# Kernel optimization log

Measured on AMD Instinct MI355X. Metric: run time of the kernel, lower is better.

Reference implementation:

```python
import jax, jax.numpy as jnp
import numpy as np

N_NODES = 50000
N_EDGES = 800000
IN_F = 128
HID_F = 128
OUT_F = 128

def safediv(a, b):
    b = jnp.where(b == 0, jnp.ones_like(b), b)
    return a / b

def setup_inputs() -> dict:
    key = jax.random.key(0)
    ks = jax.random.split(key, 8)
    h = jax.random.normal(ks[0], (N_NODES, IN_F), dtype=jnp.float32)
    ppr_weight = jax.random.uniform(ks[1], (N_EDGES,), dtype=jnp.float32)
    Qw = jax.random.normal(ks[2], (HID_F, IN_F), dtype=jnp.float32) * (1.0 / np.sqrt(IN_F))
    Qb = jnp.zeros((HID_F,), dtype=jnp.float32)
    Ww = jax.random.normal(ks[3], (OUT_F, IN_F + HID_F), dtype=jnp.float32) * (1.0 / np.sqrt(IN_F + HID_F))
    Wb = jnp.zeros((OUT_F,), dtype=jnp.float32)
    src = jax.random.randint(ks[4], (N_EDGES,), 0, N_NODES, dtype=jnp.int64 if jax.config.jax_enable_x64 else jnp.int32)
    dst = jax.random.randint(ks[5], (N_EDGES,), 0, N_NODES, dtype=jnp.int64 if jax.config.jax_enable_x64 else jnp.int32)
    return {"h": h, "ppr_weight": ppr_weight, "Qw": Qw, "Qb": Qb, "Ww": Ww, "Wb": Wb, "src": src, "dst": dst}

def reference(h, ppr_weight, Qw, Qb, Ww, Wb, src, dst):
    # neighbor transform: Q(h) -> [N, HID_F]
    hq = h @ Qw.T + Qb
    # message: h_w = hq[src] * ppr_weight  (edge-weighted gather) [E, HID_F]
    msg = hq[src] * ppr_weight[:, None]
    # reduce: scatter-sum messages and weights onto dst nodes
    h_agg = jax.ops.segment_sum(msg, dst, num_segments=N_NODES)
    w = jax.ops.segment_sum(ppr_weight, dst, num_segments=N_NODES)
    # apply: PPR-weighted mean, concat, linear, leaky_relu, L2 normalize
    h_agg = safediv(h_agg, w[:, None])
    h_concat = jnp.concatenate([h, h_agg], axis=1)
    h_new = jax.nn.leaky_relu(h_concat @ Ww.T + Wb, negative_slope=0.01)
    norm = jnp.linalg.norm(h_new, axis=1, keepdims=True)
    return safediv(h_new, norm)
```

## Files before the change

### kernel.cpp

```cpp
#include <hip/hip_runtime.h>
#include <stdint.h>

#define N_NODES 50000
#define N_EDGES 800000
#define IN_F 128
#define HID_F 128
#define OUT_F 128
#define CAT_F 256
#define N_STRIPS 3125

#define NB 64
#define NBUCK 782
#define CHUNK_E (N_EDGES / NB)
#define SLEN (NBUCK * NB)
#define BCAP 1280

typedef __bf16 bf16x8 __attribute__((ext_vector_type(8)));
typedef float f32x4 __attribute__((ext_vector_type(4)));

union BF8 {
  bf16x8 v;
  uint16_t u[8];
};

__device__ __forceinline__ uint32_t f2b(float f) {
  uint32_t u = __float_as_uint(f);
  return (u + 0x7fffu + ((u >> 16) & 1u)) >> 16;
}

__global__ void __launch_bounds__(256) prep_hist_kernel(
    const int* __restrict__ dst, int* __restrict__ G,
    const float* __restrict__ Qw, const float* __restrict__ Ww,
    uint16_t* __restrict__ QwB, uint16_t* __restrict__ WwB) {
  if (blockIdx.x < NB) {
    __shared__ int hist[NBUCK];
    for (int k = threadIdx.x; k < NBUCK; k += 256) hist[k] = 0;
    __syncthreads();
    int base = blockIdx.x * CHUNK_E;
    for (int e = base + threadIdx.x; e < base + CHUNK_E; e += 256)
      atomicAdd(&hist[dst[e] >> 6], 1);
    __syncthreads();
    for (int k = threadIdx.x; k < NBUCK; k += 256)
      G[k * NB + blockIdx.x] = hist[k];
  } else {
    const int TOT4 = (HID_F * IN_F + OUT_F * CAT_F) / 4;
    int i4 = (blockIdx.x - NB) * 256 + threadIdx.x;
    if (i4 >= TOT4) return;
    int base = i4 * 4;
    const float* src;
    uint16_t* dstp;
    int off;
    if (base < HID_F * IN_F) {
      src = Qw; dstp = QwB; off = base;
    } else {
      src = Ww; dstp = WwB; off = base - HID_F * IN_F;
    }
    float4 v = *(const float4*)(src + off);
    ushort4 o;
    o.x = (uint16_t)f2b(v.x); o.y = (uint16_t)f2b(v.y);
    o.z = (uint16_t)f2b(v.z); o.w = (uint16_t)f2b(v.w);
    *(ushort4*)(dstp + off) = o;
  }
}

__global__ void __launch_bounds__(1024) scan_kernel(const int* __restrict__ G,
                                                    int* __restrict__ offs) {
  __shared__ int wsum[17];
  int t = threadIdx.x;
  int lane = t & 63;
  int wv = t >> 6;
  int base = 0;
  for (int chunk = 0; chunk < 7; ++chunk) {
    int idx0 = chunk * 8192 + t * 8;
    int c[8];
    if (idx0 + 8 <= SLEN) {
      int4 v0 = *(const int4*)(G + idx0);
      int4 v1 = *(const int4*)(G + idx0 + 4);
      c[0] = v0.x; c[1] = v0.y; c[2] = v0.z; c[3] = v0.w;
      c[4] = v1.x; c[5] = v1.y; c[6] = v1.z; c[7] = v1.w;
    } else {
#pragma unroll
      for (int j = 0; j < 8; ++j) c[j] = (idx0 + j < SLEN) ? G[idx0 + j] : 0;
    }
    int loc[8];
    int s = 0;
#pragma unroll
    for (int j = 0; j < 8; ++j) {
      loc[j] = s;
      s += c[j];
    }
    int inc = s;
#pragma unroll
    for (int d = 1; d < 64; d <<= 1) {
      int v = __shfl_up(inc, d, 64);
      if (lane >= d) inc += v;
    }
    if (lane == 63) wsum[wv] = inc;
    __syncthreads();
    if (wv == 0) {
      int x = (lane < 16) ? wsum[lane] : 0;
      int xi = x;
#pragma unroll
      for (int d = 1; d < 16; d <<= 1) {
        int v = __shfl_up(xi, d, 64);
        if (lane >= d) xi += v;
      }
      if (lane < 16) wsum[lane] = xi - x;
      if (lane == 15) wsum[16] = xi;
    }
    __syncthreads();
    int texc = base + wsum[wv] + (inc - s);
    int ctot = wsum[16];
#pragma unroll
    for (int j = 0; j < 8; ++j) {
      int i = idx0 + j;
      if (i <= SLEN) offs[i] = texc + loc[j];
    }
    base += ctot;
    __syncthreads();
  }
}

__device__ __forceinline__ void gemm1_body(int gb, const float* __restrict__ h,
                                           const uint16_t* __restrict__ QwB,
                                           const float* __restrict__ Qb,
                                           uint16_t* __restrict__ hqB) {
  int wave = (gb * 256 + (int)threadIdx.x) >> 6;
  if (wave >= N_STRIPS) return;
  int lane = threadIdx.x & 63;
  int r = lane & 15, qd = lane >> 4;
  int row0 = wave * 16;
  f32x4 acc[8];
#pragma unroll
  for (int t = 0; t < 8; ++t) acc[t] = (f32x4){0.f, 0.f, 0.f, 0.f};
  const float* aRow = h + (size_t)(row0 + r) * IN_F + qd * 8;
#pragma unroll
  for (int kt = 0; kt < 4; ++kt) {
    float4 v0 = *(const float4*)(aRow + kt * 32);
    float4 v1 = *(const float4*)(aRow + kt * 32 + 4);
    BF8 a;
    a.u[0] = (uint16_t)f2b(v0.x); a.u[1] = (uint16_t)f2b(v0.y);
    a.u[2] = (uint16_t)f2b(v0.z); a.u[3] = (uint16_t)f2b(v0.w);
    a.u[4] = (uint16_t)f2b(v1.x); a.u[5] = (uint16_t)f2b(v1.y);
    a.u[6] = (uint16_t)f2b(v1.z); a.u[7] = (uint16_t)f2b(v1.w);
#pragma unroll
    for (int t = 0; t < 8; ++t) {
      bf16x8 b = *(const bf16x8*)(QwB + (t * 16 + r) * IN_F + kt * 32 + qd * 8);
      acc[t] = __builtin_amdgcn_mfma_f32_16x16x32_bf16(a.v, b, acc[t], 0, 0, 0);
    }
  }
#pragma unroll
  for (int t = 0; t < 8; ++t) {
    float qb = Qb[t * 16 + r];
#pragma unroll
    for (int rr = 0; rr < 4; ++rr) {
      int m = row0 + qd * 4 + rr;
      hqB[(size_t)m * HID_F + t * 16 + r] = (uint16_t)f2b(acc[t][rr] + qb);
    }
  }
}

__global__ void __launch_bounds__(256) scatter_gemm1_kernel(
    const int* __restrict__ dst, const int* __restrict__ src, const float* __restrict__ ppr,
    const int* __restrict__ offs, int2* __restrict__ rec, const float* __restrict__ h,
    const uint16_t* __restrict__ QwB, const float* __restrict__ Qb,
    uint16_t* __restrict__ hqB) {
  if (blockIdx.x < NB) {
    __shared__ int cursor[NBUCK];
    int b = blockIdx.x;
    for (int k = threadIdx.x; k < NBUCK; k += 256) cursor[k] = offs[k * NB + b];
    __syncthreads();
    int base = b * CHUNK_E;
    for (int e = base + threadIdx.x; e < base + CHUNK_E; e += 256) {
      int d = dst[e];
      int s = src[e];
      float w = ppr[e];
      int pos = atomicAdd(&cursor[d >> 6], 1);
      rec[pos] = make_int2(s | ((d & 63) << 20), __float_as_int(w));
    }
  } else {
    gemm1_body(blockIdx.x - NB, h, QwB, Qb, hqB);
  }
}

__global__ void __launch_bounds__(256) aggregate_kernel(const uint16_t* __restrict__ hqB,
                                                        const int2* __restrict__ rec,
                                                        const int* __restrict__ offs,
                                                        uint16_t* __restrict__ haggB) {
  __shared__ int2 srec[BCAP];
  __shared__ int hist[64];
  __shared__ int noff[65];
  __shared__ int cur[64];
  int g = blockIdx.x;
  int t = threadIdx.x;
  if (t < 64) hist[t] = 0;
  __syncthreads();

  int rbeg = offs[g * NB];
  int rend = offs[(g + 1) * NB];
  int len = rend - rbeg;

  for (int i = t; i < len; i += 256) {
    int2 rc = rec[rbeg + i];
    atomicAdd(&hist[rc.x >> 20], 1);
  }
  __syncthreads();

  if (t < 64) {
    int v = hist[t];
    int inc = v;
#pragma unroll
    for (int d = 1; d < 64; d <<= 1) {
      int x = __shfl_up(inc, d, 64);
      if (t >= d) inc += x;
    }
    noff[t] = inc - v;
    cur[t] = inc - v;
    if (t == 63) noff[64] = inc;
  }
  __syncthreads();

  for (int i = t; i < len; i += 256) {
    int2 rc = rec[rbeg + i];
    int p = atomicAdd(&cur[rc.x >> 20], 1);
    if (p < BCAP) srec[p] = rc;
  }
  __syncthreads();

  int lane = t & 63, wv = t >> 6;
  int sub = lane >> 4, c = lane & 15;
  const uint4* hq4 = (const uint4*)hqB;
  for (int nl = wv * 16; nl < wv * 16 + 16; ++nl) {
    int node = g * 64 + nl;
    if (node >= N_NODES) continue;
    int nbeg = noff[nl], nend = noff[nl + 1];
    int m = nend - nbeg;
    float a[8];
#pragma unroll
    for (int j = 0; j < 8; ++j) a[j] = 0.f;
    float ws = 0.f;
    if (m > 0) {
      int last = nend - 1;
      for (int e0 = nbeg; e0 < nend; e0 += 16) {
        int2 rc[4];
#pragma unroll
        for (int q = 0; q < 4; ++q) {
          int i = e0 + q * 4 + sub;
          rc[q] = srec[(i < last) ? i : last];
        }
        uint4 u[4];
#pragma unroll
        for (int q = 0; q < 4; ++q) u[q] = hq4[(size_t)(rc[q].x & 0xFFFFF) * 16 + c];
#pragma unroll
        for (int q = 0; q < 4; ++q) {
          float w = (e0 + q * 4 + sub <= last) ? __int_as_float(rc[q].y) : 0.f;
          ws += w;
          uint32_t x;
          x = u[q].x;
          a[0] += w * __uint_as_float(x << 16);
          a[1] += w * __uint_as_float(x & 0xffff0000u);
          x = u[q].y;
          a[2] += w * __uint_as_float(x << 16);
          a[3] += w * __uint_as_float(x & 0xffff0000u);
          x = u[q].z;
          a[4] += w * __uint_as_float(x << 16);
          a[5] += w * __uint_as_float(x & 0xffff0000u);
          x = u[q].w;
          a[6] += w * __uint_as_float(x << 16);
          a[7] += w * __uint_as_float(x & 0xffff0000u);
        }
      }
    }
#pragma unroll
    for (int j = 0; j < 8; ++j) {
      a[j] += __shfl_xor(a[j], 16);
      a[j] += __shfl_xor(a[j], 32);
    }
    ws += __shfl_xor(ws, 16);
    ws += __shfl_xor(ws, 32);
    float dnm = (ws == 0.f) ? 1.f : ws;
    float inv = 1.f / dnm;
    if (sub == 0) {
      uint4 o;
      o.x = f2b(a[0] * inv) | (f2b(a[1] * inv) << 16);
      o.y = f2b(a[2] * inv) | (f2b(a[3] * inv) << 16);
      o.z = f2b(a[4] * inv) | (f2b(a[5] * inv) << 16);
      o.w = f2b(a[6] * inv) | (f2b(a[7] * inv) << 16);
      ((uint4*)haggB)[(size_t)node * 16 + c] = o;
    }
  }
}

__global__ void __launch_bounds__(256) gemm2_kernel(const float* __restrict__ h,
                                                    const uint16_t* __restrict__ haggB,
                                                    const uint16_t* __restrict__ WwB,
                                                    const float* __restrict__ Wb,
                                                    float* __restrict__ out) {
  int wave = (blockIdx.x * 256 + (int)threadIdx.x) >> 6;
  if (wave >= N_STRIPS) return;
  int lane = threadIdx.x & 63;
  int r = lane & 15, qd = lane >> 4;
  int row0 = wave * 16;
  f32x4 acc[8];
#pragma unroll
  for (int t = 0; t < 8; ++t) acc[t] = (f32x4){0.f, 0.f, 0.f, 0.f};
  const float* aRow = h + (size_t)(row0 + r) * IN_F + qd * 8;
#pragma unroll
  for (int kt = 0; kt < 8; ++kt) {
    bf16x8 av;
    if (kt < 4) {
      float4 v0 = *(const float4*)(aRow + kt * 32);
      float4 v1 = *(const float4*)(aRow + kt * 32 + 4);
      BF8 ab;
      ab.u[0] = (uint16_t)f2b(v0.x); ab.u[1] = (uint16_t)f2b(v0.y);
      ab.u[2] = (uint16_t)f2b(v0.z); ab.u[3] = (uint16_t)f2b(v0.w);
      ab.u[4] = (uint16_t)f2b(v1.x); ab.u[5] = (uint16_t)f2b(v1.y);
      ab.u[6] = (uint16_t)f2b(v1.z); ab.u[7] = (uint16_t)f2b(v1.w);
      av = ab.v;
    } else {
      av = *(const bf16x8*)(haggB + (size_t)(row0 + r) * HID_F + (kt - 4) * 32 + qd * 8);
    }
#pragma unroll
    for (int t = 0; t < 8; ++t) {
      bf16x8 b = *(const bf16x8*)(WwB + (t * 16 + r) * CAT_F + kt * 32 + qd * 8);
      acc[t] = __builtin_amdgcn_mfma_f32_16x16x32_bf16(av, b, acc[t], 0, 0, 0);
    }
  }
  float lv[8][4];
  float ss[4] = {0.f, 0.f, 0.f, 0.f};
#pragma unroll
  for (int t = 0; t < 8; ++t) {
    float wb = Wb[t * 16 + r];
#pragma unroll
    for (int rr = 0; rr < 4; ++rr) {
      float v = acc[t][rr] + wb;
      v = (v >= 0.f) ? v : 0.01f * v;
      lv[t][rr] = v;
      ss[rr] += v * v;
    }
  }
#pragma unroll
  for (int rr = 0; rr < 4; ++rr) {
    float s = ss[rr];
    s += __shfl_xor(s, 1);
    s += __shfl_xor(s, 2);
    s += __shfl_xor(s, 4);
    s += __shfl_xor(s, 8);
    float nr = sqrtf(s);
    float inv = (nr == 0.f) ? 1.f : (1.f / nr);
    int mrow = row0 + qd * 4 + rr;
    float* orow = out + (size_t)mrow * OUT_F;
#pragma unroll
    for (int t = 0; t < 8; ++t) orow[t * 16 + r] = lv[t][rr] * inv;
  }
}

extern "C" void kernel_launch(void* const* d_in, const int* in_sizes, int n_in,
                              void* d_out, int out_size, void* d_ws, size_t ws_size,
                              hipStream_t stream) {
  const float* h = (const float*)d_in[0];
  const float* ppr = (const float*)d_in[1];
  const float* Qw = (const float*)d_in[2];
  const float* Qb = (const float*)d_in[3];
  const float* Ww = (const float*)d_in[4];
  const float* Wb = (const float*)d_in[5];
  const int* src = (const int*)d_in[6];
  const int* dst = (const int*)d_in[7];
  float* out = (float*)d_out;

  char* ws = (char*)d_ws;
  size_t o = 0;
  auto alloc = [&](size_t bytes) {
    void* p = ws + o;
    o = (o + bytes + 255) & ~(size_t)255;
    return p;
  };
  uint16_t* hqB = (uint16_t*)alloc((size_t)N_NODES * HID_F * 2);
  uint16_t* haggB = (uint16_t*)alloc((size_t)N_NODES * HID_F * 2);
  uint16_t* QwB = (uint16_t*)alloc((size_t)HID_F * IN_F * 2);
  uint16_t* WwB = (uint16_t*)alloc((size_t)OUT_F * CAT_F * 2);
  int* G = (int*)alloc((size_t)SLEN * 4);
  int* offs = (int*)alloc((size_t)(SLEN + 1) * 4);
  int2* rec = (int2*)alloc((size_t)N_EDGES * 8);

  prep_hist_kernel<<<NB + 48, 256, 0, stream>>>(dst, G, Qw, Ww, QwB, WwB);
  scan_kernel<<<1, 1024, 0, stream>>>(G, offs);
  scatter_gemm1_kernel<<<NB + 782, 256, 0, stream>>>(dst, src, ppr, offs, rec, h, QwB, Qb, hqB);
  aggregate_kernel<<<NBUCK, 256, 0, stream>>>(hqB, rec, offs, haggB);
  gemm2_kernel<<<(N_STRIPS * 64 + 255) / 256, 256, 0, stream>>>(h, haggB, WwB, Wb, out);
}
```

Before: 219.8 us.

## Fuse aggregation with output GEMM and split scan into parallel bucket scans

Each aggregation block now keeps its 64 aggregated node rows in LDS and runs the second GEMM, leaky ReLU and L2 normalisation directly, so the global haggB round trip and one kernel launch go away. The single-block global scan is replaced by a per-bucket wave scan plus a small base scan, and the number of scatter chunks rises from 64 to 256 to spread the scatter work over more blocks. In exchange there is one extra tiny launch, more cursor initialisation per scatter block, and extra LDS per aggregation block, which may lower occupancy.

New measurement: 190.3 us. -13.4%, faster.

```diff
diff --git a/kernel.cpp b/kernel.cpp
--- a/kernel.cpp
+++ b/kernel.cpp
@@ -9,10 +9,9 @@
 #define CAT_F 256
 #define N_STRIPS 3125
 
-#define NB 64
+#define NB 256
 #define NBUCK 782
 #define CHUNK_E (N_EDGES / NB)
-#define SLEN (NBUCK * NB)
 #define BCAP 1280
 
 typedef __bf16 bf16x8 __attribute__((ext_vector_type(8)));
@@ -63,61 +62,52 @@
   }
 }
 
-__global__ void __launch_bounds__(1024) scan_kernel(const int* __restrict__ G,
-                                                    int* __restrict__ offs) {
-  __shared__ int wsum[17];
-  int t = threadIdx.x;
-  int lane = t & 63;
-  int wv = t >> 6;
-  int base = 0;
-  for (int chunk = 0; chunk < 7; ++chunk) {
-    int idx0 = chunk * 8192 + t * 8;
-    int c[8];
-    if (idx0 + 8 <= SLEN) {
-      int4 v0 = *(const int4*)(G + idx0);
-      int4 v1 = *(const int4*)(G + idx0 + 4);
-      c[0] = v0.x; c[1] = v0.y; c[2] = v0.z; c[3] = v0.w;
-      c[4] = v1.x; c[5] = v1.y; c[6] = v1.z; c[7] = v1.w;
-    } else {
-#pragma unroll
-      for (int j = 0; j < 8; ++j) c[j] = (idx0 + j < SLEN) ? G[idx0 + j] : 0;
-    }
-    int loc[8];
-    int s = 0;
-#pragma unroll
-    for (int j = 0; j < 8; ++j) {
-      loc[j] = s;
-      s += c[j];
-    }
-    int inc = s;
-#pragma unroll
-    for (int d = 1; d < 64; d <<= 1) {
-      int v = __shfl_up(inc, d, 64);
-      if (lane >= d) inc += v;
-    }
-    if (lane == 63) wsum[wv] = inc;
-    __syncthreads();
-    if (wv == 0) {
-      int x = (lane < 16) ? wsum[lane] : 0;
-      int xi = x;
-#pragma unroll
-      for (int d = 1; d < 16; d <<= 1) {
-        int v = __shfl_up(xi, d, 64);
-        if (lane >= d) xi += v;
-      }
-      if (lane < 16) wsum[lane] = xi - x;
-      if (lane == 15) wsum[16] = xi;
-    }
-    __syncthreads();
-    int texc = base + wsum[wv] + (inc - s);
-    int ctot = wsum[16];
-#pragma unroll
-    for (int j = 0; j < 8; ++j) {
-      int i = idx0 + j;
-      if (i <= SLEN) offs[i] = texc + loc[j];
-    }
-    base += ctot;
-    __syncthreads();
+__global__ void __launch_bounds__(256) bucket_scan_kernel(const int* __restrict__ G,
+                                                          int* __restrict__ Gs,
+                                                          int* __restrict__ Btot) {
+  int w = (blockIdx.x * 256 + (int)threadIdx.x) >> 6;
+  if (w >= NBUCK) return;
+  int lane = threadIdx.x & 63;
+  int4 v = *(const int4*)(G + (size_t)w * NB + lane * 4);
+  int s = v.x + v.y + v.z + v.w;
+  int inc = s;
+#pragma unroll
+  for (int d = 1; d < 64; d <<= 1) {
+    int x = __shfl_up(inc, d, 64);
+    if (lane >= d) inc += x;
+  }
+  int exc = inc - s;
+  int4 o;
+  o.x = exc;
+  o.y = exc + v.x;
+  o.z = exc + v.x + v.y;
+  o.w = exc + v.x + v.y + v.z;
+  *(int4*)(Gs + (size_t)w * NB + lane * 4) = o;
+  if (lane == 63) Btot[w] = inc;
+}
+
+__global__ void base_scan_kernel(const int* __restrict__ Btot, int* __restrict__ Bbase) {
+  int lane = threadIdx.x;
+  int c[13], loc[13];
+  int s = 0;
+#pragma unroll
+  for (int j = 0; j < 13; ++j) {
+    int i = lane * 13 + j;
+    c[j] = (i < NBUCK) ? Btot[i] : 0;
+    loc[j] = s;
+    s += c[j];
+  }
+  int inc = s;
+#pragma unroll
+  for (int d = 1; d < 64; d <<= 1) {
+    int x = __shfl_up(inc, d, 64);
+    if (lane >= d) inc += x;
+  }
+  int exc = inc - s;
+#pragma unroll
+  for (int j = 0; j < 13; ++j) {
+    int i = lane * 13 + j;
+    if (i <= NBUCK) Bbase[i] = exc + loc[j];
   }
 }
 
@@ -162,13 +152,14 @@
 
 __global__ void __launch_bounds__(256) scatter_gemm1_kernel(
     const int* __restrict__ dst, const int* __restrict__ src, const float* __restrict__ ppr,
-    const int* __restrict__ offs, int2* __restrict__ rec, const float* __restrict__ h,
-    const uint16_t* __restrict__ QwB, const float* __restrict__ Qb,
-    uint16_t* __restrict__ hqB) {
+    const int* __restrict__ Gs, const int* __restrict__ Bbase, int2* __restrict__ rec,
+    const float* __restrict__ h, const uint16_t* __restrict__ QwB,
+    const float* __restrict__ Qb, uint16_t* __restrict__ hqB) {
   if (blockIdx.x < NB) {
     __shared__ int cursor[NBUCK];
     int b = blockIdx.x;
-    for (int k = threadIdx.x; k < NBUCK; k += 256) cursor[k] = offs[k * NB + b];
+    for (int k = threadIdx.x; k < NBUCK; k += 256)
+      cursor[k] = Bbase[k] + Gs[(size_t)k * NB + b];
     __syncthreads();
     int base = b * CHUNK_E;
     for (int e = base + threadIdx.x; e < base + CHUNK_E; e += 256) {
@@ -183,11 +174,13 @@
   }
 }
 
-__global__ void __launch_bounds__(256) aggregate_kernel(const uint16_t* __restrict__ hqB,
-                                                        const int2* __restrict__ rec,
-                                                        const int* __restrict__ offs,
-                                                        uint16_t* __restrict__ haggB) {
+__global__ void __launch_bounds__(256) agg_gemm2_kernel(
+    const uint16_t* __restrict__ hqB, const int2* __restrict__ rec,
+    const int* __restrict__ Bbase, const float* __restrict__ h,
+    const uint16_t* __restrict__ WwB, const float* __restrict__ Wb,
+    float* __restrict__ out) {
   __shared__ int2 srec[BCAP];
+  __shared__ uint4 hagg[64][17];
   __shared__ int hist[64];
   __shared__ int noff[65];
   __shared__ int cur[64];
@@ -196,8 +189,8 @@
   if (t < 64) hist[t] = 0;
   __syncthreads();
 
-  int rbeg = offs[g * NB];
-  int rend = offs[(g + 1) * NB];
+  int rbeg = Bbase[g];
+  int rend = Bbase[g + 1];
   int len = rend - rbeg;
 
   for (int i = t; i < len; i += 256) {
@@ -286,24 +279,17 @@
       o.y = f2b(a[2] * inv) | (f2b(a[3] * inv) << 16);
       o.z = f2b(a[4] * inv) | (f2b(a[5] * inv) << 16);
       o.w = f2b(a[6] * inv) | (f2b(a[7] * inv) << 16);
-      ((uint4*)haggB)[(size_t)node * 16 + c] = o;
-    }
-  }
-}
-
-__global__ void __launch_bounds__(256) gemm2_kernel(const float* __restrict__ h,
-                                                    const uint16_t* __restrict__ haggB,
-                                                    const uint16_t* __restrict__ WwB,
-                                                    const float* __restrict__ Wb,
-                                                    float* __restrict__ out) {
-  int wave = (blockIdx.x * 256 + (int)threadIdx.x) >> 6;
-  if (wave >= N_STRIPS) return;
-  int lane = threadIdx.x & 63;
+      hagg[nl][c] = o;
+    }
+  }
+  __syncthreads();
+
+  int row0 = g * 64 + wv * 16;
+  if (row0 >= N_NODES) return;
   int r = lane & 15, qd = lane >> 4;
-  int row0 = wave * 16;
   f32x4 acc[8];
 #pragma unroll
-  for (int t = 0; t < 8; ++t) acc[t] = (f32x4){0.f, 0.f, 0.f, 0.f};
+  for (int tt = 0; tt < 8; ++tt) acc[tt] = (f32x4){0.f, 0.f, 0.f, 0.f};
   const float* aRow = h + (size_t)(row0 + r) * IN_F + qd * 8;
 #pragma unroll
   for (int kt = 0; kt < 8; ++kt) {
@@ -318,24 +304,24 @@
       ab.u[6] = (uint16_t)f2b(v1.z); ab.u[7] = (uint16_t)f2b(v1.w);
       av = ab.v;
     } else {
-      av = *(const bf16x8*)(haggB + (size_t)(row0 + r) * HID_F + (kt - 4) * 32 + qd * 8);
-    }
-#pragma unroll
-    for (int t = 0; t < 8; ++t) {
-      bf16x8 b = *(const bf16x8*)(WwB + (t * 16 + r) * CAT_F + kt * 32 + qd * 8);
-      acc[t] = __builtin_amdgcn_mfma_f32_16x16x32_bf16(av, b, acc[t], 0, 0, 0);
+      av = *(const bf16x8*)&hagg[wv * 16 + r][(kt - 4) * 4 + qd];
+    }
+#pragma unroll
+    for (int tt = 0; tt < 8; ++tt) {
+      bf16x8 b = *(const bf16x8*)(WwB + (tt * 16 + r) * CAT_F + kt * 32 + qd * 8);
+      acc[tt] = __builtin_amdgcn_mfma_f32_16x16x32_bf16(av, b, acc[tt], 0, 0, 0);
     }
   }
   float lv[8][4];
   float ss[4] = {0.f, 0.f, 0.f, 0.f};
 #pragma unroll
-  for (int t = 0; t < 8; ++t) {
-    float wb = Wb[t * 16 + r];
+  for (int tt = 0; tt < 8; ++tt) {
+    float wb = Wb[tt * 16 + r];
 #pragma unroll
     for (int rr = 0; rr < 4; ++rr) {
-      float v = acc[t][rr] + wb;
+      float v = acc[tt][rr] + wb;
       v = (v >= 0.f) ? v : 0.01f * v;
-      lv[t][rr] = v;
+      lv[tt][rr] = v;
       ss[rr] += v * v;
     }
   }
@@ -351,7 +337,7 @@
     int mrow = row0 + qd * 4 + rr;
     float* orow = out + (size_t)mrow * OUT_F;
 #pragma unroll
-    for (int t = 0; t < 8; ++t) orow[t * 16 + r] = lv[t][rr] * inv;
+    for (int tt = 0; tt < 8; ++tt) orow[tt * 16 + r] = lv[tt][rr] * inv;
   }
 }
 
@@ -376,16 +362,18 @@
     return p;
   };
   uint16_t* hqB = (uint16_t*)alloc((size_t)N_NODES * HID_F * 2);
-  uint16_t* haggB = (uint16_t*)alloc((size_t)N_NODES * HID_F * 2);
   uint16_t* QwB = (uint16_t*)alloc((size_t)HID_F * IN_F * 2);
   uint16_t* WwB = (uint16_t*)alloc((size_t)OUT_F * CAT_F * 2);
-  int* G = (int*)alloc((size_t)SLEN * 4);
-  int* offs = (int*)alloc((size_t)(SLEN + 1) * 4);
+  int* G = (int*)alloc((size_t)NBUCK * NB * 4);
+  int* Gs = (int*)alloc((size_t)NBUCK * NB * 4);
+  int* Btot = (int*)alloc((size_t)NBUCK * 4);
+  int* Bbase = (int*)alloc((size_t)(NBUCK + 1) * 4);
   int2* rec = (int2*)alloc((size_t)N_EDGES * 8);
 
   prep_hist_kernel<<<NB + 48, 256, 0, stream>>>(dst, G, Qw, Ww, QwB, WwB);
-  scan_kernel<<<1, 1024, 0, stream>>>(G, offs);
-  scatter_gemm1_kernel<<<NB + 782, 256, 0, stream>>>(dst, src, ppr, offs, rec, h, QwB, Qb, hqB);
-  aggregate_kernel<<<NBUCK, 256, 0, stream>>>(hqB, rec, offs, haggB);
-  gemm2_kernel<<<(N_STRIPS * 64 + 255) / 256, 256, 0, stream>>>(h, haggB, WwB, Wb, out);
-}
+  bucket_scan_kernel<<<(NBUCK + 3) / 4, 256, 0, stream>>>(G, Gs, Btot);
+  base_scan_kernel<<<1, 64, 0, stream>>>(Btot, Bbase);
+  scatter_gemm1_kernel<<<NB + 782, 256, 0, stream>>>(dst, src, ppr, Gs, Bbase, rec, h, QwB,
+                                                     Qb, hqB);
+  agg_gemm2_kernel<<<NBUCK, 256, 0, stream>>>(hqB, rec, Bbase, h, WwB, Wb, out);
+}
```
